# Optimization experiments

Measured on AMD Instinct MI355X. Metric: run time of the kernel, lower is better.

## Reference

```python
import jax, jax.numpy as jnp
import numpy as np

EPS = 1e-10
BETA = 1.0  # beta passed to VectorQuantizer in Encoder_conv


def _conv(x, w, b, stride, pad):
    # x: NCHW, w: OIHW
    y = jax.lax.conv_general_dilated(x, w, window_strides=stride, padding=pad,
                                     dimension_numbers=('NCHW', 'OIHW', 'NCHW'))
    if b is not None:
        y = y + b[None, :, None, None]
    return y


def _forward(x, w_in, b_in, w_h1, b_h1, w_h2, b_h2, w_h3, b_h3,
             r0_w1, r0_w2, r1_w1, r1_w2, emb):
    relu = jax.nn.relu
    h = relu(_conv(x, w_in, b_in, (2, 2), [(1, 1), (1, 1)]))      # [B,128,256,256]
    h = relu(_conv(h, w_h1, b_h1, (4, 4), [(2, 2), (2, 2)]))      # [B,256,64,64]
    h = relu(_conv(h, w_h2, b_h2, (4, 4), [(2, 2), (2, 2)]))      # [B,256,16,16]
    h = relu(_conv(h, w_h3, b_h3, (2, 2), [(1, 1), (1, 1)]))      # [B,256,8,8]
    # ResidualBlock with 2 Residual layers: relu->conv[1,3]->relu->conv[1,1], no bias
    for wa, wb in ((r0_w1, r0_w2), (r1_w1, r1_w2)):
        t = _conv(relu(h), wa, None, (1, 1), [(0, 0), (1, 1)])
        t = _conv(relu(t), wb, None, (1, 1), [(0, 0), (0, 0)])
        h = h + t
    h = relu(h)
    # VectorQuantizer
    lat = jnp.transpose(h, (0, 2, 3, 1))                          # [B,H,W,D]
    D = emb.shape[1]
    flat = lat.reshape(-1, D)                                     # [N,D]
    dist = (jnp.sum(flat * flat, axis=1, keepdims=True)
            + jnp.sum(emb * emb, axis=1)
            - 2.0 * flat @ emb.T)                                 # [N,K]
    idx = jnp.argmin(dist, axis=1)                                # [N]
    quant = emb[idx].reshape(lat.shape)                           # [B,H,W,D]
    sg = jax.lax.stop_gradient
    e_loss = jnp.mean((sg(quant) - lat) ** 2)
    q_loss = jnp.mean((quant - sg(lat)) ** 2)
    loss = q_loss + BETA * e_loss
    quant_st = lat + sg(quant - lat)                              # straight-through
    probs = jnp.mean(jax.nn.one_hot(idx, emb.shape[0], dtype=lat.dtype), axis=0)
    perplexity = jnp.exp(-jnp.sum(probs * jnp.log(probs + EPS)))
    return jnp.transpose(quant_st, (0, 3, 1, 2)), loss, perplexity


def setup_inputs() -> dict:
    key = jax.random.key(0)
    ks = jax.random.split(key, 14)
    C_in, C, K = 3, 256, 512
    s = 0.05
    f32 = jnp.float32
    return {
        'x':     jax.random.normal(ks[0], (8, C_in, 512, 512), f32),
        'w_in':  jax.random.normal(ks[1], (C // 2, C_in, 4, 4), f32) * s,
        'b_in':  jnp.zeros((C // 2,), f32),
        'w_h1':  jax.random.normal(ks[2], (C, C // 2, 7, 7), f32) * s,
        'b_h1':  jnp.zeros((C,), f32),
        'w_h2':  jax.random.normal(ks[3], (C, C, 7, 7), f32) * s,
        'b_h2':  jnp.zeros((C,), f32),
        'w_h3':  jax.random.normal(ks[4], (C, C, 3, 3), f32) * s,
        'b_h3':  jnp.zeros((C,), f32),
        'r0_w1': jax.random.normal(ks[5], (4 * C, C, 1, 3), f32) * s,
        'r0_w2': jax.random.normal(ks[6], (C, 4 * C, 1, 1), f32) * s,
        'r1_w1': jax.random.normal(ks[7], (4 * C, C, 1, 3), f32) * s,
        'r1_w2': jax.random.normal(ks[8], (C, 4 * C, 1, 1), f32) * s,
        'emb':   jax.random.uniform(ks[9], (K, C), f32, -1.0 / K, 1.0 / K),
    }


def reference(x, w_in, b_in, w_h1, b_h1, w_h2, b_h2, w_h3, b_h3,
              r0_w1, r0_w2, r1_w1, r1_w2, emb):
    return _forward(x, w_in, b_in, w_h1, b_h1, w_h2, b_h2, w_h3, b_h3,
                    r0_w1, r0_w2, r1_w1, r1_w2, emb)
```

## Files before the change

### kernel.cpp

```cpp
#include <hip/hip_runtime.h>
#include <hip/hip_bf16.h>

typedef __hip_bfloat16 bf16;
typedef __attribute__((ext_vector_type(4))) float f32x4;
typedef __attribute__((ext_vector_type(8))) short short8;

__device__ __forceinline__ float b2f(bf16 v) { return __bfloat162float(v); }
__device__ __forceinline__ ushort f2bu(float v)
{
    bf16 b = __float2bfloat16(v);
    return *(ushort*)&b;
}
__device__ __forceinline__ uint relu2(uint v)
{
    uint r = v;
    if (r & 0x8000u)     r &= 0xFFFF0000u;
    if (r & 0x80000000u) r &= 0x0000FFFFu;
    return r;
}
__device__ __forceinline__ uint packbf2(float a, float b)
{
    uint lo = f2bu(a), hi = f2bu(b);
    return lo | (hi << 16);
}

typedef const __attribute__((address_space(1))) unsigned int* as1_u32;
typedef __attribute__((address_space(3))) unsigned int* as3_u32;
__device__ __forceinline__ void gld16(const void* g, uint* l)
{
    __builtin_amdgcn_global_load_lds((as1_u32)g, (as3_u32)l, 16, 0, 0);
}

__global__ __launch_bounds__(256) void initw_k(
        const float* __restrict__ w_in, const float* __restrict__ w_h1,
        const float* __restrict__ w_h2, const float* __restrict__ w_h3,
        const float* __restrict__ r0w1, const float* __restrict__ r0w2,
        const float* __restrict__ r1w1, const float* __restrict__ r1w2,
        const float* __restrict__ emb,
        bf16* __restrict__ wp1, bf16* __restrict__ wpack2, bf16* __restrict__ wpack3,
        bf16* __restrict__ wp4, bf16* __restrict__ wpA0, bf16* __restrict__ wpA1,
        bf16* __restrict__ wpB0, bf16* __restrict__ wpB1,
        float* __restrict__ en, float* __restrict__ mse, int* __restrict__ hist,
        float* __restrict__ zpad)
{
    __shared__ ushort ls[12544];
    int b = blockIdx.x, t = threadIdx.x;

    if (b < 256) {
        const float* src = w_h1 + (size_t)b * 6272;
        for (int i = t; i < 6272; i += 256) ls[i] = f2bu(src[i]);
        __syncthreads();
        for (int e = t; e < 800; e += 256) {
            int tap = e >> 4, cib8 = e & 15;
            short8 v;
            #pragma unroll
            for (int cil = 0; cil < 8; ++cil)
                v[cil] = (tap < 49) ? (short)ls[(cib8 * 8 + cil) * 49 + tap] : (short)0;
            *(short8*)(wpack2 + ((size_t)(tap * 16 + cib8) * 256 + b) * 8) = v;
        }
        return;
    }
    if (b < 512) {
        int co = b - 256;
        const float* src = w_h2 + (size_t)co * 12544;
        for (int i = t; i < 12544; i += 256) ls[i] = f2bu(src[i]);
        __syncthreads();
        for (int e = t; e < 1600; e += 256) {
            int tap = e >> 5, cib8 = e & 31;
            short8 v;
            #pragma unroll
            for (int cil = 0; cil < 8; ++cil)
                v[cil] = (tap < 49) ? (short)ls[(cib8 * 8 + cil) * 49 + tap] : (short)0;
            *(short8*)(wpack3 + ((size_t)(tap * 32 + cib8) * 256 + co) * 8) = v;
        }
        return;
    }
    if (b < 768) {
        int co = b - 512;
        const float* src = w_h3 + (size_t)co * 2304;
        for (int i = t; i < 2304; i += 256) ls[i] = f2bu(src[i]);
        __syncthreads();
        for (int e = t; e < 288; e += 256) {
            int tap = e >> 5, cib8 = e & 31;
            short8 v;
            #pragma unroll
            for (int cil = 0; cil < 8; ++cil)
                v[cil] = (short)ls[(cib8 * 8 + cil) * 9 + tap];
            *(short8*)(wp4 + ((size_t)(tap * 32 + cib8) * 256 + co) * 8) = v;
        }
        return;
    }
    if (b < 2816) {
        int r = b - 768;
        int which = r >> 10;
        int co = r & 1023;
        const float* srcb = which ? r1w1 : r0w1;
        bf16* dstb = which ? wpA1 : wpA0;
        const float* src = srcb + (size_t)co * 768;
        for (int i = t; i < 768; i += 256) ls[i] = f2bu(src[i]);
        __syncthreads();
        if (t < 96) {
            int tap = t >> 5, cib8 = t & 31;
            short8 v;
            #pragma unroll
            for (int cil = 0; cil < 8; ++cil)
                v[cil] = (short)ls[(cib8 * 8 + cil) * 3 + tap];
            *(short8*)(dstb + ((size_t)(tap * 32 + cib8) * 1024 + co) * 8) = v;
        }
        return;
    }
    if (b < 3072) {
        int r = b - 2816;
        int which = r >> 7;
        const float* srcb = which ? r1w2 : r0w2;
        bf16* dstb = which ? wpB1 : wpB0;
        int c = (r & 127) * 256 + t;
        int cib8 = c >> 8, co = c & 255;
        const float* s = srcb + (size_t)co * 1024 + cib8 * 8;
        short8 v;
        #pragma unroll
        for (int cil = 0; cil < 8; ++cil) v[cil] = (short)f2bu(s[cil]);
        *(short8*)(dstb + (size_t)c * 8) = v;
        return;
    }
    if (b < 3104) {
        int i = (b - 3072) * 256 + t;
        int j = i & 7; int co = (i >> 3) & 127; int kb = i >> 10;
        int k = kb * 8 + j;
        wp1[i] = __float2bfloat16(k < 48 ? w_in[co * 48 + k] : 0.f);
        return;
    }
    if (b < 3106) {
        int row = (b - 3104) * 256 + t;
        const float4* e = (const float4*)(emb + (size_t)row * 256);
        float s = 0.f;
        for (int d4 = 0; d4 < 64; ++d4) {
            float4 v = e[d4];
            s += v.x * v.x + v.y * v.y + v.z * v.z + v.w * v.w;
        }
        en[row] = s;
        return;
    }
    if (t == 0) mse[0] = 0.f;
    for (int i = t; i < 512; i += 256) hist[i] = 0;
    if (t < 64) zpad[t] = 0.f;
}

__global__ __launch_bounds__(256) void conv1m_k(const float* __restrict__ x,
        const bf16* __restrict__ wp1, const float* __restrict__ bias,
        bf16* __restrict__ h1c)
{
    int bid = blockIdx.x;
    int pxt = bid & 511, img = bid >> 9;
    int tr = pxt >> 4, tc = pxt & 15;
    int oh0 = tr * 8, ow0 = tc * 16;
    const float* xi = x + (size_t)img * 786432;
    bf16* oT = h1c + (size_t)img * 8388608;

    int t = threadIdx.x;
    int wave = t >> 6, lane = t & 63;
    int quad = lane >> 4, l15 = lane & 15;

    __shared__ ushort xs[4 * 640];
    __shared__ ushort ot[128 * 136];

    int ihb = oh0 * 2 - 1, iwb = ow0 * 2 - 1;
    for (int i = t; i < 1836; i += 256) {
        int ci = i / 612; int r1 = i - ci * 612;
        int ihl = r1 / 34, iwl = r1 - ihl * 34;
        int ih = ihb + ihl, iw = iwb + iwl;
        float v = 0.f;
        if ((unsigned)ih < 512u && (unsigned)iw < 512u)
            v = xi[ci * 262144 + ih * 512 + iw];
        xs[ci * 640 + ihl * 35 + iwl] = f2bu(v);
    }
    for (int i = t; i < 640; i += 256) xs[3 * 640 + i] = 0;
    __syncthreads();

    f32x4 zero = {0.f, 0.f, 0.f, 0.f};
    f32x4 acc[8][2];
    #pragma unroll
    for (int m = 0; m < 8; ++m) { acc[m][0] = zero; acc[m][1] = zero; }

    int ci_b = quad >> 1;
    int kh0 = (quad & 1) * 2;
    int iwl0 = 2 * l15;

    #pragma unroll
    for (int ks = 0; ks < 2; ++ks) {
        union { short8 v; uint u[4]; } b[2];
        #pragma unroll
        for (int nt = 0; nt < 2; ++nt) {
            int py = wave * 2 + nt;
            int base = (ks * 2 + ci_b) * 640 + (2 * py + kh0) * 35 + iwl0;
            b[nt].u[0] = *(const uint*)&xs[base];
            b[nt].u[1] = *(const uint*)&xs[base + 2];
            b[nt].u[2] = *(const uint*)&xs[base + 35];
            b[nt].u[3] = *(const uint*)&xs[base + 37];
        }
        const bf16* abase = wp1 + ((size_t)(ks * 4 + quad) * 128 + l15) * 8;
        #pragma unroll
        for (int m = 0; m < 8; ++m) {
            short8 a = *(const short8*)(abase + m * 16 * 8);
            acc[m][0] = __builtin_amdgcn_mfma_f32_16x16x32_bf16(a, b[0].v, acc[m][0], 0, 0, 0);
            acc[m][1] = __builtin_amdgcn_mfma_f32_16x16x32_bf16(a, b[1].v, acc[m][1], 0, 0, 0);
        }
    }

    #pragma unroll
    for (int m = 0; m < 8; ++m) {
        int cobase = m * 16 + quad * 4;
        float b0 = bias[cobase], b1 = bias[cobase + 1];
        float b2 = bias[cobase + 2], b3 = bias[cobase + 3];
        #pragma unroll
        for (int nt = 0; nt < 2; ++nt) {
            int pxl = (wave * 2 + nt) * 16 + l15;
            uint w0 = packbf2(fmaxf(b0 + acc[m][nt][0], 0.f),
                              fmaxf(b1 + acc[m][nt][1], 0.f));
            uint w1 = packbf2(fmaxf(b2 + acc[m][nt][2], 0.f),
                              fmaxf(b3 + acc[m][nt][3], 0.f));
            *(uint*)&ot[pxl * 136 + cobase]     = w0;
            *(uint*)&ot[pxl * 136 + cobase + 2] = w1;
        }
    }
    __syncthreads();
    {
        int pxl = t >> 1, half = t & 1;
        int oh = oh0 + (pxl >> 4), ow = ow0 + (pxl & 15);
        size_t px = (size_t)(oh * 256 + ow);
        #pragma unroll
        for (int cb = 0; cb < 4; ++cb) {
            int c16 = half * 4 + cb;
            const uint4* src = (const uint4*)&ot[pxl * 136 + c16 * 16];
            uint4* dst = (uint4*)(oT + ((size_t)c16 * 65536 + px) * 16);
            dst[0] = src[0];
            dst[1] = src[1];
        }
    }
}

template <int IH, int OH, int CI, int SPLIT, int MODE>
__global__ __launch_bounds__(256, 2) void conv_mfma8_k(
        const bf16* __restrict__ inC, const bf16* __restrict__ wpack,
        const float* __restrict__ bias, float* __restrict__ outA,
        bf16* __restrict__ outT, const float* __restrict__ zpad)
{
    constexpr int TPD = OH / 8;
    constexpr int NT = TPD * TPD;
    constexpr int CPB = (CI / 16) / SPLIT;
    constexpr int CIB8 = CI / 8;
    constexpr int NPX = IH * IH;
    constexpr int SLOTS = 2496;

    int bid = blockIdx.x;
    int pxt = bid % NT;
    int rest = bid / NT;
    int img = rest & 7;
    int split = rest >> 3;
    int oh0 = (pxt / TPD) * 8, ow0 = (pxt % TPD) * 8;

    int t = threadIdx.x;
    int wave = t >> 6, lane = t & 63;
    int quad = lane >> 4, l15 = lane & 15;
    int pxh = wave >> 1, coh = wave & 1;

    const bf16* inb = inC + (size_t)img * ((size_t)NPX * CI);

    __shared__ __align__(16) uint bufA[SLOTS * 4];
    __shared__ __align__(16) uint bufB[SLOTS * 4];

    f32x4 zero = {0.f, 0.f, 0.f, 0.f};
    f32x4 acc[8][2];
    #pragma unroll
    for (int a = 0; a < 8; ++a) {
        acc[a][0] = zero; acc[a][1] = zero;
    }

    int ihb = oh0 * 4 - 2, iwb = ow0 * 4 - 2;
    int qxl = l15 & 7, pyl = l15 >> 3;
    int tap_par = quad >> 1, ci_half = quad & 1;

    int  srel[10];
    bool sval[10];
    #pragma unroll
    for (int it = 0; it < 10; ++it) {
        int sb = (it < 9) ? it * 256 + wave * 64 : 2304 + wave * 64;
        int p  = sb + lane;
        int pb = p << 4;
        int lb = pb ^ (((pb >> 7) & 7) << 4);
        int j  = lb >> 4;
        int pos = j >> 1, half = j & 1;
        int r = pos / 35, c = pos - r * 35;
        int ih = ihb + r, iw = iwb + c;
        sval[it] = (j < 2450) && ((unsigned)ih < (unsigned)IH)
                   && ((unsigned)iw < (unsigned)IH);
        srel[it] = (ih * IH + iw) * 16 + half * 8;
    }

    auto stage = [&](int ch, uint* dst) {
        const bf16* cbp = inb + (size_t)ch * NPX * 16;
        #pragma unroll
        for (int it = 0; it < 10; ++it) {
            if (it == 9 && wave >= 3) continue;
            int sb = (it < 9) ? it * 256 + wave * 64 : 2304 + wave * 64;
            const void* src = sval[it] ? (const void*)(cbp + srel[it])
                                       : (const void*)zpad;
            gld16(src, dst + sb * 4);
        }
    };

    int rbase = pxh * 17920 + pyl * 4480 + qxl * 128 + ci_half * 16;
    int d1  = tap_par * 32;
    int d29 = tap_par * 928;

    auto compute = [&](int ch, const uint* cbuf) {
        const bf16* ab = wpack
            + ((size_t)(ch * 2 + ci_half) * 256 + coh * 128 + l15) * 8
            + (size_t)tap_par * (CIB8 * 2048);
        __builtin_amdgcn_s_setprio(1);
        #pragma unroll
        for (int tp = 0; tp < 25; ++tp) {
            const int kh0 = (2 * tp) / 7, kw0 = (2 * tp) % 7;
            const int cE  = (kh0 * 35 + kw0) * 32;
            int dsel = (tp == 24) ? 0 : ((kw0 == 6) ? d29 : d1);
            int lbb  = rbase + cE + dsel;
            const bf16* at = ab + (size_t)(2 * tp) * (CIB8 * 2048);
            short8 a[8];
            #pragma unroll
            for (int ct = 0; ct < 8; ++ct)
                a[ct] = *(const short8*)(at + ct * 128);
            #pragma unroll
            for (int pt = 0; pt < 2; ++pt) {
                int lb = lbb + pt * 8960;
                int pb = lb ^ (((lb >> 7) & 7) << 4);
                short8 b = *(const short8*)((const char*)cbuf + pb);
                #pragma unroll
                for (int ct = 0; ct < 8; ++ct)
                    acc[ct][pt] = __builtin_amdgcn_mfma_f32_16x16x32_bf16(
                        a[ct], b, acc[ct][pt], 0, 0, 0);
            }
        }
        __builtin_amdgcn_s_setprio(0);
    };

    stage(split * CPB, bufA);
    __syncthreads();
    for (int cc2 = 0; cc2 < CPB; cc2 += 2) {
        stage(split * CPB + cc2 + 1, bufB);
        compute(split * CPB + cc2, bufA);
        __syncthreads();
        if (cc2 + 2 < CPB) stage(split * CPB + cc2 + 2, bufA);
        compute(split * CPB + cc2 + 1, bufB);
        __syncthreads();
    }

    #pragma unroll
    for (int ct = 0; ct < 8; ++ct) {
        int cobase = coh * 128 + ct * 16 + quad * 4;
        #pragma unroll
        for (int pt = 0; pt < 2; ++pt) {
            int px = pxh * 32 + pt * 16 + l15;
            int oh = oh0 + (px >> 3), ow = ow0 + (px & 7);
            int pxg = oh * OH + ow;
            #pragma unroll
            for (int r = 0; r < 4; ++r) {
                int co = cobase + r;
                float v = acc[ct][pt][r];
                if (MODE == 3) {
                    outA[(size_t)split * ((size_t)8 * OH * OH * 256)
                         + (size_t)img * (OH * OH * 256)
                         + (size_t)co * (OH * OH) + pxg] = v;
                } else {
                    float o = fmaxf(bias[co] + v, 0.f);
                    size_t base = (size_t)img * (size_t)(OH * OH * 256);
                    outT[base + ((size_t)(co >> 4) * (OH * OH) + pxg) * 16 + (co & 15)]
                        = __float2bfloat16(o);
                }
            }
        }
    }
}

__global__ void combine3_k(const float* __restrict__ p3, const float* __restrict__ bias,
                           bf16* __restrict__ h3T)
{
    int idx = blockIdx.x * 256 + threadIdx.x;
    int px = idx & 255;
    int co = (idx >> 8) & 255;
    int img = idx >> 16;
    float v = bias[co];
    #pragma unroll
    for (int s = 0; s < 8; ++s) v += p3[(size_t)s * 524288 + idx];
    v = fmaxf(v, 0.f);
    h3T[((size_t)img * 256 + px) * 256 + co] = __float2bfloat16(v);
}

__global__ __launch_bounds__(256) void conv4m_k(const bf16* __restrict__ h3T,
        const bf16* __restrict__ wp4, const float* __restrict__ bias,
        bf16* __restrict__ h4T)
{
    int bid = blockIdx.x;
    int img = bid >> 2, cog = bid & 3;
    int t = threadIdx.x;
    int wave = t >> 6, lane = t & 63;
    int quad = lane >> 4, l15 = lane & 15;

    __shared__ uint pt[16 * 325];

    for (int i = t; i < 16 * 325; i += 256) pt[i] = 0;

    f32x4 zero = {0.f, 0.f, 0.f, 0.f};
    f32x4 acc[4];
    #pragma unroll
    for (int b = 0; b < 4; ++b) acc[b] = zero;

    const bf16* inb = h3T + (size_t)img * 65536;

    for (int ch = 0; ch < 8; ++ch) {
        __syncthreads();
        for (int e = t; e < 4096; e += 256) {
            int cp = e & 15, px = e >> 4;
            int py = px >> 4, qx = px & 15;
            uint v = *(const uint*)(inb + (size_t)px * 256 + ch * 32 + cp * 2);
            pt[cp * 325 + (py + 1) * 18 + qx + 1] = v;
        }
        __syncthreads();

        for (int tap = 0; tap < 9; ++tap) {
            int kh = tap / 3, kw = tap - kh * 3;
            const bf16* abase = wp4 + ((size_t)((tap * 32 + ch * 4 + quad) * 256)
                                       + cog * 64 + wave * 16 + l15) * 8;
            short8 a = *(const short8*)abase;
            #pragma unroll
            for (int pq = 0; pq < 4; ++pq) {
                int pyo = 2 * pq + (l15 >> 3);
                int ipos = (2 * pyo + kh) * 18 + 2 * (l15 & 7) + kw;
                union { short8 v; uint u[4]; } b;
                b.u[0] = pt[(quad * 4 + 0) * 325 + ipos];
                b.u[1] = pt[(quad * 4 + 1) * 325 + ipos];
                b.u[2] = pt[(quad * 4 + 2) * 325 + ipos];
                b.u[3] = pt[(quad * 4 + 3) * 325 + ipos];
                acc[pq] = __builtin_amdgcn_mfma_f32_16x16x32_bf16(
                    a, b.v, acc[pq], 0, 0, 0);
            }
        }
    }

    int cobase = cog * 64 + wave * 16 + quad * 4;
    #pragma unroll
    for (int pq = 0; pq < 4; ++pq) {
        int px = pq * 16 + l15;
        #pragma unroll
        for (int r = 0; r < 4; ++r) {
            int co = cobase + r;
            float v = fmaxf(bias[co] + acc[pq][r], 0.f);
            h4T[((size_t)img * 64 + px) * 256 + co] = __float2bfloat16(v);
        }
    }
}

__global__ __launch_bounds__(256) void resam_k(const bf16* __restrict__ hT,
        const bf16* __restrict__ wpA, bf16* __restrict__ t1T)
{
    int bid = blockIdx.x;
    int img = bid >> 3, g = bid & 7;
    int t = threadIdx.x;
    int wave = t >> 6, lane = t & 63;
    int quad = lane >> 4, l15 = lane & 15;

    __shared__ uint ph[128 * 81];

    for (int i = t; i < 128 * 81; i += 256) ph[i] = 0;
    __syncthreads();
    const bf16* inb = hT + (size_t)img * 16384;
    for (int e = t; e < 8192; e += 256) {
        int cp = e & 127, px = e >> 7;
        uint v = relu2(*(const uint*)(inb + (size_t)px * 256 + cp * 2));
        ph[cp * 81 + (px >> 3) * 10 + (px & 7) + 1] = v;
    }
    __syncthreads();

    f32x4 zero = {0.f, 0.f, 0.f, 0.f};
    f32x4 acc[2][4];
    #pragma unroll
    for (int a = 0; a < 2; ++a)
        #pragma unroll
        for (int b = 0; b < 4; ++b) acc[a][b] = zero;

    for (int ch = 0; ch < 8; ++ch) {
        for (int tap = 0; tap < 3; ++tap) {
            const bf16* abase = wpA + ((size_t)(tap * 32 + ch * 4 + quad) * 1024
                                       + g * 128 + wave * 32 + l15) * 8;
            short8 a[2];
            #pragma unroll
            for (int ct = 0; ct < 2; ++ct)
                a[ct] = *(const short8*)(abase + ct * 16 * 8);
            #pragma unroll
            for (int pq = 0; pq < 4; ++pq) {
                int py = 2 * pq + (l15 >> 3);
                int pos = py * 10 + (l15 & 7) + tap;
                union { short8 v; uint u[4]; } b;
                b.u[0] = ph[(ch * 16 + quad * 4 + 0) * 81 + pos];
                b.u[1] = ph[(ch * 16 + quad * 4 + 1) * 81 + pos];
                b.u[2] = ph[(ch * 16 + quad * 4 + 2) * 81 + pos];
                b.u[3] = ph[(ch * 16 + quad * 4 + 3) * 81 + pos];
                #pragma unroll
                for (int ct = 0; ct < 2; ++ct)
                    acc[ct][pq] = __builtin_amdgcn_mfma_f32_16x16x32_bf16(
                        a[ct], b.v, acc[ct][pq], 0, 0, 0);
            }
        }
    }

    #pragma unroll
    for (int ct = 0; ct < 2; ++ct) {
        int cobase = g * 128 + wave * 32 + ct * 16 + quad * 4;
        #pragma unroll
        for (int pq = 0; pq < 4; ++pq) {
            int px = pq * 16 + l15;
            #pragma unroll
            for (int r = 0; r < 4; ++r)
                t1T[((size_t)img * 64 + px) * 1024 + cobase + r]
                    = __float2bfloat16(acc[ct][pq][r]);
        }
    }
}

__global__ __launch_bounds__(256) void resbm_k(const bf16* __restrict__ holdT,
        const bf16* __restrict__ t1T, const bf16* __restrict__ wpB,
        bf16* __restrict__ hnewT)
{
    int bid = blockIdx.x;
    int img = bid >> 2, cog = bid & 3;
    int t = threadIdx.x;
    int wave = t >> 6, lane = t & 63;
    int quad = lane >> 4, l15 = lane & 15;

    __shared__ uint pb[256 * 65];

    f32x4 zero = {0.f, 0.f, 0.f, 0.f};
    f32x4 acc[4];
    #pragma unroll
    for (int b = 0; b < 4; ++b) acc[b] = zero;

    const bf16* inb = t1T + (size_t)img * 65536;

    for (int s = 0; s < 2; ++s) {
        __syncthreads();
        for (int e = t; e < 16384; e += 256) {
            int cp = e & 255, px = e >> 8;
            uint v = relu2(*(const uint*)(inb + (size_t)px * 1024 + s * 512 + cp * 2));
            pb[cp * 65 + px] = v;
        }
        __syncthreads();

        for (int chl = 0; chl < 16; ++chl) {
            int ch = s * 16 + chl;
            const bf16* abase = wpB + ((size_t)(ch * 4 + quad) * 256
                                       + cog * 64 + wave * 16 + l15) * 8;
            short8 a = *(const short8*)abase;
            #pragma unroll
            for (int pq = 0; pq < 4; ++pq) {
                int px = pq * 16 + l15;
                union { short8 v; uint u[4]; } b;
                b.u[0] = pb[(chl * 16 + quad * 4 + 0) * 65 + px];
                b.u[1] = pb[(chl * 16 + quad * 4 + 1) * 65 + px];
                b.u[2] = pb[(chl * 16 + quad * 4 + 2) * 65 + px];
                b.u[3] = pb[(chl * 16 + quad * 4 + 3) * 65 + px];
                acc[pq] = __builtin_amdgcn_mfma_f32_16x16x32_bf16(
                    a, b.v, acc[pq], 0, 0, 0);
            }
        }
    }

    int cobase = cog * 64 + wave * 16 + quad * 4;
    #pragma unroll
    for (int pq = 0; pq < 4; ++pq) {
        int px = pq * 16 + l15;
        #pragma unroll
        for (int r = 0; r < 4; ++r) {
            int co = cobase + r;
            size_t o = ((size_t)img * 64 + px) * 256 + co;
            float v = b2f(holdT[o]) + acc[pq][r];
            hnewT[o] = __float2bfloat16(v);
        }
    }
}

__global__ __launch_bounds__(256) void vq_k(const bf16* __restrict__ h6T,
        const float* __restrict__ emb, const float* __restrict__ en,
        float* __restrict__ out, float* __restrict__ mse_acc, int* __restrict__ hist)
{
    int row0 = blockIdx.x * 4;
    int t = threadIdx.x;
    int wave = t >> 6, lane = t & 63;
    __shared__ float lat[4][256];
    __shared__ float swd[4][4];
    __shared__ int   swi[4][4];
    __shared__ int   fidx[4];
    __shared__ float smse[4];

    for (int e = t; e < 1024; e += 256) {
        int r = e >> 8, c = e & 255;
        lat[r][c] = fmaxf(b2f(h6T[(size_t)(row0 + r) * 256 + c]), 0.f);
    }
    __syncthreads();

    float a0[4] = {0.f, 0.f, 0.f, 0.f}, a1[4] = {0.f, 0.f, 0.f, 0.f};
    const float4* e0 = (const float4*)(emb + (size_t)t * 256);
    const float4* e1 = (const float4*)(emb + (size_t)(t + 256) * 256);
    for (int d4 = 0; d4 < 64; ++d4) {
        float4 v0 = e0[d4], v1 = e1[d4];
        #pragma unroll
        for (int r = 0; r < 4; ++r) {
            float l0 = lat[r][d4 * 4], l1 = lat[r][d4 * 4 + 1];
            float l2 = lat[r][d4 * 4 + 2], l3 = lat[r][d4 * 4 + 3];
            a0[r] += l0 * v0.x + l1 * v0.y + l2 * v0.z + l3 * v0.w;
            a1[r] += l0 * v1.x + l1 * v1.y + l2 * v1.z + l3 * v1.w;
        }
    }
    float en0 = en[t], en1 = en[t + 256];
    float bd[4]; int bi[4];
    #pragma unroll
    for (int r = 0; r < 4; ++r) {
        float d0 = en0 - 2.f * a0[r], d1v = en1 - 2.f * a1[r];
        bd[r] = d0; bi[r] = t;
        if (d1v < bd[r]) { bd[r] = d1v; bi[r] = t + 256; }
    }
    #pragma unroll
    for (int s = 1; s < 64; s <<= 1) {
        #pragma unroll
        for (int r = 0; r < 4; ++r) {
            float od = __shfl_xor(bd[r], s);
            int   oi = __shfl_xor(bi[r], s);
            if (od < bd[r] || (od == bd[r] && oi < bi[r])) { bd[r] = od; bi[r] = oi; }
        }
    }
    if (lane == 0) {
        #pragma unroll
        for (int r = 0; r < 4; ++r) { swd[wave][r] = bd[r]; swi[wave][r] = bi[r]; }
    }
    __syncthreads();
    if (t < 4) {
        float best = swd[0][t]; int bidx = swi[0][t];
        for (int w = 1; w < 4; ++w) {
            float od = swd[w][t]; int oi = swi[w][t];
            if (od < best || (od == best && oi < bidx)) { best = od; bidx = oi; }
        }
        fidx[t] = bidx;
    }
    __syncthreads();

    float msel = 0.f;
    #pragma unroll
    for (int r = 0; r < 4; ++r) {
        int row = row0 + r;
        int b = row >> 6, y = (row >> 3) & 7, xx = row & 7;
        float q = emb[(size_t)fidx[r] * 256 + t];
        out[((size_t)(b * 256 + t) * 8 + y) * 8 + xx] = q;
        float diff = q - lat[r][t];
        msel += diff * diff;
    }
    #pragma unroll
    for (int s = 1; s < 64; s <<= 1) msel += __shfl_xor(msel, s);
    if (lane == 0) smse[wave] = msel;
    __syncthreads();
    if (t == 0) atomicAdd(mse_acc, smse[0] + smse[1] + smse[2] + smse[3]);
    if (t < 4) atomicAdd(&hist[fidx[t]], 1);
}

__global__ void final_k(const float* __restrict__ mse_acc, const int* __restrict__ hist,
                        float* __restrict__ out)
{
    __shared__ float sh[512];
    int t = threadIdx.x;
    float p = (float)hist[t] / 512.f;
    sh[t] = p * logf(p + 1e-10f);
    __syncthreads();
    for (int s = 256; s > 0; s >>= 1) {
        if (t < s) sh[t] += sh[t + s];
        __syncthreads();
    }
    if (t == 0) {
        float loss = 2.f * mse_acc[0] / (512.f * 256.f);
        float perp = expf(-sh[0]);
        out[131072] = loss;
        out[131073] = perp;
    }
}

extern "C" void kernel_launch(void* const* d_in, const int* in_sizes, int n_in,
                              void* d_out, int out_size, void* d_ws, size_t ws_size,
                              hipStream_t stream)
{
    const float* x    = (const float*)d_in[0];
    const float* w_in = (const float*)d_in[1];
    const float* b_in = (const float*)d_in[2];
    const float* w_h1 = (const float*)d_in[3];
    const float* b_h1 = (const float*)d_in[4];
    const float* w_h2 = (const float*)d_in[5];
    const float* b_h2 = (const float*)d_in[6];
    const float* w_h3 = (const float*)d_in[7];
    const float* b_h3 = (const float*)d_in[8];
    const float* r0w1 = (const float*)d_in[9];
    const float* r0w2 = (const float*)d_in[10];
    const float* r1w1 = (const float*)d_in[11];
    const float* r1w2 = (const float*)d_in[12];
    const float* emb  = (const float*)d_in[13];
    float* out = (float*)d_out;

    char* ws = (char*)d_ws;
    size_t off = 0;
    auto alloc = [&](size_t bytes) -> void* {
        void* p = ws + off;
        off += (bytes + 255) & ~(size_t)255;
        return p;
    };

    float* en  = (float*)alloc(512 * 4);
    float* mse = (float*)alloc(256);
    int*  hist = (int*)alloc(512 * 4);
    float* zpad = (float*)alloc(256);
    float* p3  = (float*)alloc(4194304ull * 4);
    bf16* h3T  = (bf16*)alloc(524288ull * 2);
    bf16* h4T  = (bf16*)alloc(131072ull * 2);
    bf16* t1T  = (bf16*)alloc(524288ull * 2);
    bf16* h5T  = (bf16*)alloc(131072ull * 2);
    bf16* h6T  = (bf16*)alloc(131072ull * 2);
    bf16* wp1  = (bf16*)alloc(8192ull * 2);
    bf16* wpack2 = (bf16*)alloc(1638400ull * 2);
    bf16* wpack3 = (bf16*)alloc(3276800ull * 2);
    bf16* wp4  = (bf16*)alloc(589824ull * 2);
    bf16* wpA0 = (bf16*)alloc(786432ull * 2);
    bf16* wpA1 = (bf16*)alloc(786432ull * 2);
    bf16* wpB0 = (bf16*)alloc(262144ull * 2);
    bf16* wpB1 = (bf16*)alloc(262144ull * 2);
    bf16* h2c  = (bf16*)alloc(8388608ull * 2);
    size_t base_end = off;

    const size_t H1F_B = 8388608ull * 8 * 2;
    size_t needT1 = base_end + H1F_B + 4096;
    bf16* h1c;
    int tier;
    if (ws_size >= needT1) {
        h1c = (bf16*)alloc(H1F_B);
        tier = 1;
    } else {
        h1c = (bf16*)alloc(8388608ull * 2);
        tier = 2;
    }

    initw_k<<<3107, 256, 0, stream>>>(w_in, w_h1, w_h2, w_h3, r0w1, r0w2, r1w1, r1w2,
        emb, wp1, wpack2, wpack3, wp4, wpA0, wpA1, wpB0, wpB1, en, mse, hist, zpad);

    if (tier == 1) {
        conv1m_k<<<4096, 256, 0, stream>>>(x, wp1, b_in, h1c);
        conv_mfma8_k<256, 64, 128, 1, 0><<<512, 256, 0, stream>>>(
            h1c, wpack2, b_h1, nullptr, h2c, zpad);
    } else {
        for (int n = 0; n < 8; ++n) {
            conv1m_k<<<512, 256, 0, stream>>>(x + (size_t)n * 786432, wp1, b_in, h1c);
            conv_mfma8_k<256, 64, 128, 1, 0><<<64, 256, 0, stream>>>(
                h1c, wpack2, b_h1, nullptr, h2c + (size_t)n * 1048576, zpad);
        }
    }

    conv_mfma8_k<64, 16, 256, 8, 3><<<256, 256, 0, stream>>>(
        h2c, wpack3, nullptr, p3, nullptr, zpad);
    combine3_k<<<2048, 256, 0, stream>>>(p3, b_h2, h3T);

    conv4m_k<<<32, 256, 0, stream>>>(h3T, wp4, b_h3, h4T);
    resam_k<<<64, 256, 0, stream>>>(h4T, wpA0, t1T);
    resbm_k<<<32, 256, 0, stream>>>(h4T, t1T, wpB0, h5T);
    resam_k<<<64, 256, 0, stream>>>(h5T, wpA1, t1T);
    resbm_k<<<32, 256, 0, stream>>>(h5T, t1T, wpB1, h6T);

    vq_k<<<128, 256, 0, stream>>>(h6T, emb, en, out, mse, hist);
    final_k<<<1, 512, 0, stream>>>(mse, hist, out);
}
```

Before: 471.5 us.

## Retile conv MFMA kernel to 4x4 per wave with register prefetch and split-16

Changes each wave's tile from 128 output channels by 32 pixels to 64 channels by all 64 pixels, so per tap it issues 4 A-loads and 4 B-loads for 16 MFMAs. Loads for the next tap are double-buffered in registers so they can overlap the current tap's MFMAs. For the conv3 layer it doubles the channel split from 8 to 16, giving 512 blocks with one chunk each, and adds a single-chunk path that skips the ping-pong staging. The cost is a larger fp32 partial buffer, a heavier combine pass reading 16 partials, and more register pressure from the prefetch.

```diff
diff --git a/kernel.cpp b/kernel.cpp
--- a/kernel.cpp
+++ b/kernel.cpp
@@ -240,7 +240,7 @@
 }
 
 template <int IH, int OH, int CI, int SPLIT, int MODE>
-__global__ __launch_bounds__(256, 2) void conv_mfma8_k(
+__global__ __launch_bounds__(256, 2) void conv_mfma9_k(
         const bf16* __restrict__ inC, const bf16* __restrict__ wpack,
         const float* __restrict__ bias, float* __restrict__ outA,
         bf16* __restrict__ outT, const float* __restrict__ zpad)
@@ -262,7 +262,6 @@
     int t = threadIdx.x;
     int wave = t >> 6, lane = t & 63;
     int quad = lane >> 4, l15 = lane & 15;
-    int pxh = wave >> 1, coh = wave & 1;
 
     const bf16* inb = inC + (size_t)img * ((size_t)NPX * CI);
 
@@ -270,11 +269,11 @@
     __shared__ __align__(16) uint bufB[SLOTS * 4];
 
     f32x4 zero = {0.f, 0.f, 0.f, 0.f};
-    f32x4 acc[8][2];
-    #pragma unroll
-    for (int a = 0; a < 8; ++a) {
-        acc[a][0] = zero; acc[a][1] = zero;
-    }
+    f32x4 acc[4][4];
+    #pragma unroll
+    for (int a = 0; a < 4; ++a)
+        #pragma unroll
+        for (int b = 0; b < 4; ++b) acc[a][b] = zero;
 
     int ihb = oh0 * 4 - 2, iwb = ow0 * 4 - 2;
     int qxl = l15 & 7, pyl = l15 >> 3;
@@ -309,57 +308,84 @@
         }
     };
 
-    int rbase = pxh * 17920 + pyl * 4480 + qxl * 128 + ci_half * 16;
+    int rbase = pyl * 4480 + qxl * 128 + ci_half * 16;
     int d1  = tap_par * 32;
     int d29 = tap_par * 928;
 
     auto compute = [&](int ch, const uint* cbuf) {
         const bf16* ab = wpack
-            + ((size_t)(ch * 2 + ci_half) * 256 + coh * 128 + l15) * 8
+            + ((size_t)(ch * 2 + ci_half) * 256 + wave * 64 + l15) * 8
             + (size_t)tap_par * (CIB8 * 2048);
         __builtin_amdgcn_s_setprio(1);
-        #pragma unroll
-        for (int tp = 0; tp < 25; ++tp) {
-            const int kh0 = (2 * tp) / 7, kw0 = (2 * tp) % 7;
-            const int cE  = (kh0 * 35 + kw0) * 32;
-            int dsel = (tp == 24) ? 0 : ((kw0 == 6) ? d29 : d1);
-            int lbb  = rbase + cE + dsel;
-            const bf16* at = ab + (size_t)(2 * tp) * (CIB8 * 2048);
-            short8 a[8];
-            #pragma unroll
-            for (int ct = 0; ct < 8; ++ct)
-                a[ct] = *(const short8*)(at + ct * 128);
-            #pragma unroll
-            for (int pt = 0; pt < 2; ++pt) {
+        short8 aC[4], bC[4], aN[4], bN[4];
+        {
+            #pragma unroll
+            for (int ct = 0; ct < 4; ++ct)
+                aC[ct] = *(const short8*)(ab + ct * 128);
+            int lbb = rbase + d1;
+            #pragma unroll
+            for (int pt = 0; pt < 4; ++pt) {
                 int lb = lbb + pt * 8960;
                 int pb = lb ^ (((lb >> 7) & 7) << 4);
-                short8 b = *(const short8*)((const char*)cbuf + pb);
+                bC[pt] = *(const short8*)((const char*)cbuf + pb);
+            }
+        }
+        #pragma unroll
+        for (int tp = 0; tp < 25; ++tp) {
+            if (tp < 24) {
+                const int tn  = tp + 1;
+                const int kh0 = (2 * tn) / 7, kw0 = (2 * tn) % 7;
+                const int cE  = (kh0 * 35 + kw0) * 32;
+                int dsel = (tn == 24) ? 0 : ((kw0 == 6) ? d29 : d1);
+                int lbb  = rbase + cE + dsel;
+                const bf16* at = ab + (size_t)(2 * tn) * (CIB8 * 2048);
                 #pragma unroll
-                for (int ct = 0; ct < 8; ++ct)
+                for (int ct = 0; ct < 4; ++ct)
+                    aN[ct] = *(const short8*)(at + ct * 128);
+                #pragma unroll
+                for (int pt = 0; pt < 4; ++pt) {
+                    int lb = lbb + pt * 8960;
+                    int pb = lb ^ (((lb >> 7) & 7) << 4);
+                    bN[pt] = *(const short8*)((const char*)cbuf + pb);
+                }
+            }
+            #pragma unroll
+            for (int pt = 0; pt < 4; ++pt)
+                #pragma unroll
+                for (int ct = 0; ct < 4; ++ct)
                     acc[ct][pt] = __builtin_amdgcn_mfma_f32_16x16x32_bf16(
-                        a[ct], b, acc[ct][pt], 0, 0, 0);
+                        aC[ct], bC[pt], acc[ct][pt], 0, 0, 0);
+            if (tp < 24) {
+                #pragma unroll
+                for (int i = 0; i < 4; ++i) { aC[i] = aN[i]; bC[i] = bN[i]; }
             }
         }
         __builtin_amdgcn_s_setprio(0);
     };
 
-    stage(split * CPB, bufA);
-    __syncthreads();
-    for (int cc2 = 0; cc2 < CPB; cc2 += 2) {
-        stage(split * CPB + cc2 + 1, bufB);
-        compute(split * CPB + cc2, bufA);
-        __syncthreads();
-        if (cc2 + 2 < CPB) stage(split * CPB + cc2 + 2, bufA);
-        compute(split * CPB + cc2 + 1, bufB);
-        __syncthreads();
-    }
-
-    #pragma unroll
-    for (int ct = 0; ct < 8; ++ct) {
-        int cobase = coh * 128 + ct * 16 + quad * 4;
-        #pragma unroll
-        for (int pt = 0; pt < 2; ++pt) {
-            int px = pxh * 32 + pt * 16 + l15;
+    if constexpr (CPB == 1) {
+        stage(split, bufA);
+        __syncthreads();
+        compute(split, bufA);
+    } else {
+        stage(split * CPB, bufA);
+        __syncthreads();
+        for (int cc2 = 0; cc2 < CPB; cc2 += 2) {
+            stage(split * CPB + cc2 + 1, bufB);
+            compute(split * CPB + cc2, bufA);
+            __syncthreads();
+            if (cc2 + 2 < CPB) stage(split * CPB + cc2 + 2, bufA);
+            compute(split * CPB + cc2 + 1, bufB);
+            __syncthreads();
+        }
+    }
+
+    #pragma unroll
+    for (int ct = 0; ct < 4; ++ct) {
+        int cobase = wave * 64 + ct * 16 + quad * 4;
+        #pragma unroll
+        for (int pt = 0; pt < 4; ++pt) {
+            int px = pt * 16 + l15;
             int oh = oh0 + (px >> 3), ow = ow0 + (px & 7);
             int pxg = oh * OH + ow;
             #pragma unroll
@@ -390,7 +416,7 @@
     int img = idx >> 16;
     float v = bias[co];
     #pragma unroll
-    for (int s = 0; s < 8; ++s) v += p3[(size_t)s * 524288 + idx];
+    for (int s = 0; s < 16; ++s) v += p3[(size_t)s * 524288 + idx];
     v = fmaxf(v, 0.f);
     h3T[((size_t)img * 256 + px) * 256 + co] = __float2bfloat16(v);
 }
@@ -721,7 +747,7 @@
     float* mse = (float*)alloc(256);
     int*  hist = (int*)alloc(512 * 4);
     float* zpad = (float*)alloc(256);
-    float* p3  = (float*)alloc(4194304ull * 4);
+    float* p3  = (float*)alloc(8388608ull * 4);
     bf16* h3T  = (bf16*)alloc(524288ull * 2);
     bf16* h4T  = (bf16*)alloc(131072ull * 2);
     bf16* t1T  = (bf16*)alloc(524288ull * 2);
@@ -755,17 +781,17 @@
 
     if (tier == 1) {
         conv1m_k<<<4096, 256, 0, stream>>>(x, wp1, b_in, h1c);
-        conv_mfma8_k<256, 64, 128, 1, 0><<<512, 256, 0, stream>>>(
+        conv_mfma9_k<256, 64, 128, 1, 0><<<512, 256, 0, stream>>>(
             h1c, wpack2, b_h1, nullptr, h2c, zpad);
     } else {
         for (int n = 0; n < 8; ++n) {
             conv1m_k<<<512, 256, 0, stream>>>(x + (size_t)n * 786432, wp1, b_in, h1c);
-            conv_mfma8_k<256, 64, 128, 1, 0><<<64, 256, 0, stream>>>(
+            conv_mfma9_k<256, 64, 128, 1, 0><<<64, 256, 0, stream>>>(
                 h1c, wpack2, b_h1, nullptr, h2c + (size_t)n * 1048576, zpad);
         }
     }
 
-    conv_mfma8_k<64, 16, 256, 8, 3><<<256, 256, 0, stream>>>(
+    conv_mfma9_k<64, 16, 256, 16, 3><<<512, 256, 0, stream>>>(
         h2c, wpack3, nullptr, p3, nullptr, zpad);
     combine3_k<<<2048, 256, 0, stream>>>(p3, b_h2, h3T);
 
```

Result: no change. 464.4 us (-1.5%).
